# Kernel tuning notes

Measured on AMD Instinct MI355X. Metric: run time of the kernel, lower is better.

Reference implementation:

```python
import jax, jax.numpy as jnp
import numpy as np

D_MODEL = 1024
NUM_HEADS = 16
HEAD_DIM = D_MODEL // NUM_HEADS


def setup_inputs() -> dict:
    key = jax.random.key(0)
    ks = jax.random.split(key, 7)
    B, S = 4, 2048
    scale = 1.0 / np.sqrt(D_MODEL)
    x = jax.random.normal(ks[0], (B, S, D_MODEL), dtype=jnp.float32)
    Wq = jax.random.normal(ks[1], (D_MODEL, D_MODEL), dtype=jnp.float32) * scale
    Wk = jax.random.normal(ks[2], (D_MODEL, D_MODEL), dtype=jnp.float32) * scale
    Wv = jax.random.normal(ks[3], (D_MODEL, D_MODEL), dtype=jnp.float32) * scale
    bq = jax.random.normal(ks[4], (D_MODEL,), dtype=jnp.float32) * 0.02
    bk = jax.random.normal(ks[5], (D_MODEL,), dtype=jnp.float32) * 0.02
    bv = jax.random.normal(ks[6], (D_MODEL,), dtype=jnp.float32) * 0.02
    return {"x": x, "Wq": Wq, "bq": bq, "Wk": Wk, "bk": bk, "Wv": Wv, "bv": bv}


def reference(x, Wq, bq, Wk, bk, Wv, bv):
    B, S, _ = x.shape
    # QKV projections (nn.Linear: x @ W^T + b; here W stored as [in, out] already)
    q = x @ Wq + bq
    k = x @ Wk + bk
    v = x @ Wv + bv
    # [B, H, S, Dh]
    def split_heads(t):
        return t.reshape(B, S, NUM_HEADS, HEAD_DIM).transpose(0, 2, 1, 3)
    q, k, v = split_heads(q), split_heads(k), split_heads(v)
    # NOTE: module scales by sqrt(d_model), NOT sqrt(head_dim)
    scores = jnp.einsum("bhqd,bhkd->bhqk", q, k) / jnp.sqrt(jnp.float32(D_MODEL))
    attn = jax.nn.softmax(scores, axis=-1)  # dropout = identity (eval mode)
    out = jnp.einsum("bhqk,bhkd->bhqd", attn, v)
    return out.transpose(0, 2, 1, 3).reshape(B, S, D_MODEL)
```

## Files before the change

### kernel.cpp

```cpp
#include <hip/hip_runtime.h>


typedef __attribute__((ext_vector_type(8))) __bf16 bf16x8;
typedef __attribute__((ext_vector_type(8))) unsigned short ushort8;
typedef __attribute__((ext_vector_type(4))) float floatx4;

#if __has_builtin(__builtin_amdgcn_exp2f)
#define EXP2(x) __builtin_amdgcn_exp2f(x)
#else
#define EXP2(x) __expf((x) * 0.6931471805599453f)
#endif

__device__ __forceinline__ unsigned short f2bf(float f) {
    __bf16 h = (__bf16)f;
    return __builtin_bit_cast(unsigned short, h);
}
__device__ __forceinline__ bf16x8 pack8(floatx4 a, floatx4 b) {
    bf16x8 v = {(__bf16)a[0], (__bf16)a[1], (__bf16)a[2], (__bf16)a[3],
                (__bf16)b[0], (__bf16)b[1], (__bf16)b[2], (__bf16)b[3]};
    return v;
}
__device__ __forceinline__ floatx4 mfma16(bf16x8 a, bf16x8 b, floatx4 c) {
    return __builtin_amdgcn_mfma_f32_16x16x32_bf16(a, b, c, 0, 0, 0);
}
__device__ __forceinline__ int spos(int s) {
    int rk = s & 31;
    return (s & ~31) | (((rk & 15) >> 2) * 8 + ((rk >> 4) << 2) + (rk & 3));
}
__device__ __forceinline__ void glds16(const void* g, void* l) {
    __builtin_amdgcn_global_load_lds(
        (const __attribute__((address_space(1))) unsigned int*)g,
        (__attribute__((address_space(3))) unsigned int*)l, 16, 0, 0);
}

__global__ __launch_bounds__(256) void prep_x(const float* __restrict__ X,
                                              unsigned short* __restrict__ Xb) {
    int i = (blockIdx.x * 256 + threadIdx.x) * 8;
    float4 a = *(const float4*)&X[i];
    float4 b = *(const float4*)&X[i + 4];
    bf16x8 v = {(__bf16)a.x, (__bf16)a.y, (__bf16)a.z, (__bf16)a.w,
                (__bf16)b.x, (__bf16)b.y, (__bf16)b.z, (__bf16)b.w};
    *(bf16x8*)&Xb[i] = v;
}

__global__ __launch_bounds__(256) void prep_wt(
    const float* __restrict__ Wq, const float* __restrict__ Wk,
    const float* __restrict__ Wv,
    unsigned short* __restrict__ WqT, unsigned short* __restrict__ WkT,
    unsigned short* __restrict__ WvT) {
    __shared__ unsigned short Ls[64 * 72];
    const int tid = threadIdx.x, z = blockIdx.z;
    const float* W = (z == 0) ? Wq : (z == 1) ? Wk : Wv;
    unsigned short* WT = (z == 0) ? WqT : (z == 1) ? WkT : WvT;
    const int k0 = (blockIdx.x >> 4) * 64, o0 = (blockIdx.x & 15) * 64;
#pragma unroll
    for (int e = 0; e < 4; ++e) {
        int idx = e * 256 + tid;
        int r = idx >> 4, c = (idx & 15) * 4;
        float4 f = *(const float4*)&W[(size_t)(k0 + r) * 1024 + o0 + c];
        Ls[(c + 0) * 72 + r] = f2bf(f.x);
        Ls[(c + 1) * 72 + r] = f2bf(f.y);
        Ls[(c + 2) * 72 + r] = f2bf(f.z);
        Ls[(c + 3) * 72 + r] = f2bf(f.w);
    }
    __syncthreads();
#pragma unroll
    for (int e = 0; e < 2; ++e) {
        int idx = e * 256 + tid;
        int rr = idx >> 3, ch = (idx & 7) * 8;
        *(ushort8*)&WT[(size_t)(o0 + rr) * 1024 + k0 + ch] =
            *(const ushort8*)&Ls[rr * 72 + ch];
    }
}

__global__ __launch_bounds__(256, 3) void qkv_gemm(
    const unsigned short* __restrict__ Xb,
    const unsigned short* __restrict__ WqT,
    const unsigned short* __restrict__ WkT,
    const unsigned short* __restrict__ WvT,
    const float* __restrict__ bq, const float* __restrict__ bk,
    const float* __restrict__ bv,
    unsigned short* __restrict__ Kh, unsigned short* __restrict__ Vt,
    float* __restrict__ Qs_out) {

    __shared__ __align__(16) unsigned char arena[32768];

    const int tid = threadIdx.x;
    const int w = tid >> 6, lane = tid & 63;
    const int l15 = lane & 15, quad = lane >> 4;
    const int z = blockIdx.z;
    const int tok_base = blockIdx.x * 128, o_base = blockIdx.y * 128;
    const int wr = w >> 1, wc = w & 1;

    const unsigned short* Wsrc = (z == 0) ? WkT : (z == 1) ? WvT : WqT;
    const char* Asrc = (z == 1) ? (const char*)(Wsrc + (size_t)o_base * 1024)
                                : (const char*)(Xb + (size_t)tok_base * 1024);
    const char* Bsrc = (z == 1) ? (const char*)(Xb + (size_t)tok_base * 1024)
                                : (const char*)(Wsrc + (size_t)o_base * 1024);

    const int coff = (((lane & 7) ^ (lane >> 3)) << 4);
    const char* pa[4];
    const char* pb[4];
    unsigned char* la[4];
    unsigned char* lb[4];
#pragma unroll
    for (int e = 0; e < 4; ++e) {
        int r = (e * 4 + w) * 8 + (lane >> 3);
        pa[e] = Asrc + (size_t)r * 2048 + coff;
        pb[e] = Bsrc + (size_t)r * 2048 + coff;
        la[e] = arena + (e * 4 + w) * 1024;
        lb[e] = arena + 16384 + (e * 4 + w) * 1024;
    }

    const unsigned cq = (unsigned)((quad ^ (l15 & 7)) << 4);
    unsigned offA[4], offB[4];
#pragma unroll
    for (int t = 0; t < 4; ++t) {
        offA[t] = (unsigned)((wr * 64 + t * 16 + l15) * 128) + cq;
        offB[t] = 16384u + (unsigned)((wc * 64 + t * 16 + l15) * 128) + cq;
    }

    floatx4 acc[4][4];
#pragma unroll
    for (int mt = 0; mt < 4; ++mt)
#pragma unroll
        for (int nt = 0; nt < 4; ++nt) acc[mt][nt] = (floatx4){0.f, 0.f, 0.f, 0.f};

    for (int k0 = 0; k0 < 1024; k0 += 64) {
        __syncthreads();
#pragma unroll
        for (int e = 0; e < 4; ++e) {
            glds16(pa[e], la[e]);
            glds16(pb[e], lb[e]);
            pa[e] += 128;
            pb[e] += 128;
        }
        __syncthreads();

#pragma unroll
        for (int kc = 0; kc < 2; ++kc) {
            bf16x8 af[4], bfr[4];
#pragma unroll
            for (int mt = 0; mt < 4; ++mt)
                af[mt] = *(const bf16x8*)&arena[offA[mt] ^ (unsigned)(kc << 6)];
#pragma unroll
            for (int nt = 0; nt < 4; ++nt)
                bfr[nt] = *(const bf16x8*)&arena[offB[nt] ^ (unsigned)(kc << 6)];
#pragma unroll
            for (int mt = 0; mt < 4; ++mt)
#pragma unroll
                for (int nt = 0; nt < 4; ++nt)
                    acc[mt][nt] = mfma16(af[mt], bfr[nt], acc[mt][nt]);
        }
    }

    if (z == 0) {
#pragma unroll
        for (int nt = 0; nt < 4; ++nt) {
            int col = o_base + wc * 64 + nt * 16 + l15;
            float bia = bk[col];
            int h = col >> 6, dh = col & 63;
#pragma unroll
            for (int mt = 0; mt < 4; ++mt)
#pragma unroll
                for (int r = 0; r < 4; ++r) {
                    int t = tok_base + wr * 64 + mt * 16 + quad * 4 + r;
                    int bb = t >> 11, s = t & 2047;
                    Kh[(((size_t)(bb * 16 + h)) * 2048 + s) * 64 + dh] =
                        f2bf(acc[mt][nt][r] + bia);
                }
        }
    } else if (z == 1) {
#pragma unroll
        for (int mt = 0; mt < 4; ++mt)
#pragma unroll
            for (int r = 0; r < 4; ++r) {
                int o = o_base + wr * 64 + mt * 16 + quad * 4 + r;
                float bia = bv[o];
#pragma unroll
                for (int nt = 0; nt < 4; ++nt) {
                    int t = tok_base + wc * 64 + nt * 16 + l15;
                    int bb = t >> 11, s = t & 2047;
                    Vt[((size_t)(bb * 1024 + o)) * 2048 + spos(s)] =
                        f2bf(acc[mt][nt][r] + bia);
                }
            }
    } else {
        const float QS = 0.03125f * 1.44269504f;
#pragma unroll
        for (int nt = 0; nt < 4; ++nt) {
            int col = o_base + wc * 64 + nt * 16 + l15;
            float bia = bq[col];
#pragma unroll
            for (int mt = 0; mt < 4; ++mt)
#pragma unroll
                for (int r = 0; r < 4; ++r) {
                    int t = tok_base + wr * 64 + mt * 16 + quad * 4 + r;
                    Qs_out[(size_t)t * 1024 + col] = (acc[mt][nt][r] + bia) * QS;
                }
        }
    }
}

__global__ __launch_bounds__(256, 4) void attn_kernel(
    const unsigned short* __restrict__ Kh,
    const unsigned short* __restrict__ Vt,
    float* __restrict__ out) {

    __shared__ __align__(16) unsigned char arena[32768];

    const int tid = threadIdx.x;
    const int w = tid >> 6, lane = tid & 63;
    const int l15 = lane & 15, quad = lane >> 4;
    const int qb = blockIdx.x, h = blockIdx.y, b = blockIdx.z;
    const size_t head_elems = ((size_t)(b * 16 + h)) * 2048 * 64;

    bf16x8 aq[2][2];
#pragma unroll
    for (int g = 0; g < 2; ++g)
#pragma unroll
        for (int kc = 0; kc < 2; ++kc) {
            const float* qp = out +
                (size_t)(b * 2048 + qb * 128 + w * 32 + g * 16 + l15) * 1024 +
                h * 64 + kc * 32 + quad * 8;
            floatx4 x0 = *(const floatx4*)qp;
            floatx4 x1 = *(const floatx4*)(qp + 4);
            aq[g][kc] = pack8(x0, x1);
        }
    __builtin_amdgcn_sched_barrier(0);

    const int coff = (((lane & 7) ^ (lane >> 3)) << 4);
    const char* pk[2];
    const char* pv[2];
    unsigned char* lk[2];
    unsigned char* lv[2];
#pragma unroll
    for (int e = 0; e < 2; ++e) {
        int r = (e * 4 + w) * 8 + (lane >> 3);
        pk[e] = (const char*)Kh + head_elems * 2 + (size_t)r * 128 + coff;
        pv[e] = (const char*)Vt + ((size_t)(b * 1024 + h * 64 + r)) * 4096 + coff;
        lk[e] = arena + (e * 4 + w) * 1024;
        lv[e] = arena + 8192 + (e * 4 + w) * 1024;
    }
    auto stage = [&](int bufsel) {
        int bo = bufsel << 14;
#pragma unroll
        for (int e = 0; e < 2; ++e) {
            glds16(pk[e], lk[e] + bo);
            glds16(pv[e], lv[e] + bo);
            pk[e] += 8192;
            pv[e] += 128;
        }
    };

    unsigned kb[4], vb[4];
#pragma unroll
    for (int t = 0; t < 4; ++t) {
        int rk = t * 16 + l15;
        unsigned sw = (unsigned)((quad ^ (rk & 7)) << 4);
        kb[t] = (unsigned)(rk * 128) + sw;
        vb[t] = 8192u + (unsigned)(rk * 128) + sw;
    }

    float l_part[2] = {0.f, 0.f};
    floatx4 O[2][4];
#pragma unroll
    for (int g = 0; g < 2; ++g)
#pragma unroll
        for (int n4 = 0; n4 < 4; ++n4) O[g][n4] = (floatx4){0.f, 0.f, 0.f, 0.f};

    stage(0);

#pragma unroll 1
    for (int kt = 0; kt < 32; ++kt) {
        if (kt < 31) {
            stage((kt + 1) & 1);
            asm volatile("s_waitcnt vmcnt(4)" ::: "memory");
        } else {
            asm volatile("s_waitcnt vmcnt(0)" ::: "memory");
        }
        __builtin_amdgcn_s_barrier();
        const unsigned bsel = (unsigned)((kt & 1) << 14);

        bf16x8 ap[2][2];
#pragma unroll
        for (int kg = 0; kg < 2; ++kg) {
            floatx4 s0[2], s1[2];
#pragma unroll
            for (int mm = 0; mm < 2; ++mm) {
                int m16 = 2 * kg + mm;
                unsigned ka = kb[m16] ^ bsel;
                bf16x8 kf0 = *(const bf16x8*)&arena[ka];
                bf16x8 kf1 = *(const bf16x8*)&arena[ka ^ 64u];
#pragma unroll
                for (int g = 0; g < 2; ++g) {
                    floatx4 a0 = (floatx4){0.f, 0.f, 0.f, 0.f};
                    a0 = mfma16(kf0, aq[g][0], a0);
                    a0 = mfma16(kf1, aq[g][1], a0);
                    if (mm == 0) s0[g] = a0; else s1[g] = a0;
                }
            }
#pragma unroll
            for (int g = 0; g < 2; ++g) {
                floatx4 p0, p1;
#pragma unroll
                for (int r = 0; r < 4; ++r) {
                    p0[r] = EXP2(fminf(s0[g][r], 43.28f));
                    p1[r] = EXP2(fminf(s1[g][r], 43.28f));
                }
                l_part[g] += (p0[0] + p0[1]) + (p0[2] + p0[3]) +
                             (p1[0] + p1[1]) + (p1[2] + p1[3]);
                ap[g][kg] = pack8(p0, p1);
            }
        }

#pragma unroll
        for (int n4 = 0; n4 < 4; ++n4)
#pragma unroll
            for (int kg = 0; kg < 2; ++kg) {
                bf16x8 vf = *(const bf16x8*)
                    &arena[(vb[n4] ^ bsel) ^ (unsigned)(kg << 6)];
#pragma unroll
                for (int g = 0; g < 2; ++g)
                    O[g][n4] = mfma16(ap[g][kg], vf, O[g][n4]);
            }

        asm volatile("s_waitcnt lgkmcnt(0)" ::: "memory");
        __builtin_amdgcn_s_barrier();
    }

#pragma unroll
    for (int g = 0; g < 2; ++g) {
        float l = l_part[g];
        l += __shfl_xor(l, 16);
        l += __shfl_xor(l, 32);
#pragma unroll
        for (int r = 0; r < 4; ++r) {
            float lr = __shfl(l, (lane & 48) | (quad * 4 + r));
            float inv = 1.f / lr;
            int srow = qb * 128 + w * 32 + g * 16 + quad * 4 + r;
#pragma unroll
            for (int n4 = 0; n4 < 4; ++n4)
                out[((size_t)(b * 2048 + srow)) * 1024 + h * 64 + n4 * 16 + l15] =
                    O[g][n4][r] * inv;
        }
    }
}

extern "C" void kernel_launch(void* const* d_in, const int* in_sizes, int n_in,
                              void* d_out, int out_size, void* d_ws, size_t ws_size,
                              hipStream_t stream) {
    const float *x, *Wq, *bq, *Wk, *bk, *Wv, *bv;
    x = (const float*)d_in[0];
    if (in_sizes[2] == 1024) {
        Wq = (const float*)d_in[1];  bq = (const float*)d_in[2];
        Wk = (const float*)d_in[3];  bk = (const float*)d_in[4];
        Wv = (const float*)d_in[5];  bv = (const float*)d_in[6];
    } else {
        Wq = (const float*)d_in[1];  Wk = (const float*)d_in[2];
        Wv = (const float*)d_in[3];
        bq = (const float*)d_in[4];  bk = (const float*)d_in[5];
        bv = (const float*)d_in[6];
    }
    float* out = (float*)d_out;

    char* ws = (char*)d_ws;
    unsigned short* Xb  = (unsigned short*)(ws);
    unsigned short* Kh  = (unsigned short*)(ws + (16u << 20));
    unsigned short* Vt  = (unsigned short*)(ws + (32u << 20));
    unsigned short* WqT = (unsigned short*)(ws + (48u << 20));
    unsigned short* WkT = (unsigned short*)(ws + (50u << 20));
    unsigned short* WvT = (unsigned short*)(ws + (52u << 20));

    prep_x<<<4096, 256, 0, stream>>>(x, Xb);
    prep_wt<<<dim3(256, 1, 3), 256, 0, stream>>>(Wq, Wk, Wv, WqT, WkT, WvT);
    qkv_gemm<<<dim3(64, 8, 3), 256, 0, stream>>>(Xb, WqT, WkT, WvT, bq, bk, bv,
                                                 Kh, Vt, out);
    attn_kernel<<<dim3(16, 16, 4), 256, 0, stream>>>(Kh, Vt, out);
}
```

Measured before the change: 232.0 us.

## Merge prep kernels, compute softmax row sums via MFMA, add wave priorities

Folds the x conversion and weight transpose kernels into one launch split by block index, removing a kernel boundary. In attention, the per-row sum of exponentials now comes from an MFMA against a ones vector on the bf16-packed probabilities instead of scalar adds plus cross-lane shuffles. It also wraps the MFMA sections in s_setprio and drops the fminf clamp before exp2. Removing the clamp risks overflow if scores get large, and summing bf16-rounded probabilities slightly changes the normalisation.

```diff
diff --git a/kernel.cpp b/kernel.cpp
--- a/kernel.cpp
+++ b/kernel.cpp
@@ -33,26 +33,28 @@
         (__attribute__((address_space(3))) unsigned int*)l, 16, 0, 0);
 }
 
-__global__ __launch_bounds__(256) void prep_x(const float* __restrict__ X,
-                                              unsigned short* __restrict__ Xb) {
-    int i = (blockIdx.x * 256 + threadIdx.x) * 8;
-    float4 a = *(const float4*)&X[i];
-    float4 b = *(const float4*)&X[i + 4];
-    bf16x8 v = {(__bf16)a.x, (__bf16)a.y, (__bf16)a.z, (__bf16)a.w,
-                (__bf16)b.x, (__bf16)b.y, (__bf16)b.z, (__bf16)b.w};
-    *(bf16x8*)&Xb[i] = v;
-}
-
-__global__ __launch_bounds__(256) void prep_wt(
+__global__ __launch_bounds__(256) void prep_all(
+    const float* __restrict__ X, unsigned short* __restrict__ Xb,
     const float* __restrict__ Wq, const float* __restrict__ Wk,
     const float* __restrict__ Wv,
     unsigned short* __restrict__ WqT, unsigned short* __restrict__ WkT,
     unsigned short* __restrict__ WvT) {
     __shared__ unsigned short Ls[64 * 72];
-    const int tid = threadIdx.x, z = blockIdx.z;
+    const int tid = threadIdx.x, bx = blockIdx.x;
+    if (bx < 4096) {
+        int i = (bx * 256 + tid) * 8;
+        float4 a = *(const float4*)&X[i];
+        float4 b = *(const float4*)&X[i + 4];
+        bf16x8 v = {(__bf16)a.x, (__bf16)a.y, (__bf16)a.z, (__bf16)a.w,
+                    (__bf16)b.x, (__bf16)b.y, (__bf16)b.z, (__bf16)b.w};
+        *(bf16x8*)&Xb[i] = v;
+        return;
+    }
+    const int idx4 = bx - 4096;
+    const int z = idx4 >> 8, xx = idx4 & 255;
     const float* W = (z == 0) ? Wq : (z == 1) ? Wk : Wv;
     unsigned short* WT = (z == 0) ? WqT : (z == 1) ? WkT : WvT;
-    const int k0 = (blockIdx.x >> 4) * 64, o0 = (blockIdx.x & 15) * 64;
+    const int k0 = (xx >> 4) * 64, o0 = (xx & 15) * 64;
 #pragma unroll
     for (int e = 0; e < 4; ++e) {
         int idx = e * 256 + tid;
@@ -262,12 +264,16 @@
         vb[t] = 8192u + (unsigned)(rk * 128) + sw;
     }
 
-    float l_part[2] = {0.f, 0.f};
+    const bf16x8 ONES = {(__bf16)1.f, (__bf16)1.f, (__bf16)1.f, (__bf16)1.f,
+                         (__bf16)1.f, (__bf16)1.f, (__bf16)1.f, (__bf16)1.f};
+    floatx4 lacc[2];
     floatx4 O[2][4];
 #pragma unroll
-    for (int g = 0; g < 2; ++g)
+    for (int g = 0; g < 2; ++g) {
+        lacc[g] = (floatx4){0.f, 0.f, 0.f, 0.f};
 #pragma unroll
         for (int n4 = 0; n4 < 4; ++n4) O[g][n4] = (floatx4){0.f, 0.f, 0.f, 0.f};
+    }
 
     stage(0);
 
@@ -286,6 +292,7 @@
 #pragma unroll
         for (int kg = 0; kg < 2; ++kg) {
             floatx4 s0[2], s1[2];
+            __builtin_amdgcn_s_setprio(1);
 #pragma unroll
             for (int mm = 0; mm < 2; ++mm) {
                 int m16 = 2 * kg + mm;
@@ -300,20 +307,21 @@
                     if (mm == 0) s0[g] = a0; else s1[g] = a0;
                 }
             }
+            __builtin_amdgcn_s_setprio(0);
 #pragma unroll
             for (int g = 0; g < 2; ++g) {
                 floatx4 p0, p1;
 #pragma unroll
                 for (int r = 0; r < 4; ++r) {
-                    p0[r] = EXP2(fminf(s0[g][r], 43.28f));
-                    p1[r] = EXP2(fminf(s1[g][r], 43.28f));
-                }
-                l_part[g] += (p0[0] + p0[1]) + (p0[2] + p0[3]) +
-                             (p1[0] + p1[1]) + (p1[2] + p1[3]);
+                    p0[r] = EXP2(s0[g][r]);
+                    p1[r] = EXP2(s1[g][r]);
+                }
                 ap[g][kg] = pack8(p0, p1);
+                lacc[g] = mfma16(ap[g][kg], ONES, lacc[g]);
             }
         }
 
+        __builtin_amdgcn_s_setprio(1);
 #pragma unroll
         for (int n4 = 0; n4 < 4; ++n4)
 #pragma unroll
@@ -324,27 +332,23 @@
                 for (int g = 0; g < 2; ++g)
                     O[g][n4] = mfma16(ap[g][kg], vf, O[g][n4]);
             }
+        __builtin_amdgcn_s_setprio(0);
 
         asm volatile("s_waitcnt lgkmcnt(0)" ::: "memory");
         __builtin_amdgcn_s_barrier();
     }
 
 #pragma unroll
-    for (int g = 0; g < 2; ++g) {
-        float l = l_part[g];
-        l += __shfl_xor(l, 16);
-        l += __shfl_xor(l, 32);
+    for (int g = 0; g < 2; ++g)
 #pragma unroll
         for (int r = 0; r < 4; ++r) {
-            float lr = __shfl(l, (lane & 48) | (quad * 4 + r));
-            float inv = 1.f / lr;
+            float inv = 1.f / lacc[g][r];
             int srow = qb * 128 + w * 32 + g * 16 + quad * 4 + r;
 #pragma unroll
             for (int n4 = 0; n4 < 4; ++n4)
                 out[((size_t)(b * 2048 + srow)) * 1024 + h * 64 + n4 * 16 + l15] =
                     O[g][n4][r] * inv;
         }
-    }
 }
 
 extern "C" void kernel_launch(void* const* d_in, const int* in_sizes, int n_in,
@@ -372,8 +376,7 @@
     unsigned short* WkT = (unsigned short*)(ws + (50u << 20));
     unsigned short* WvT = (unsigned short*)(ws + (52u << 20));
 
-    prep_x<<<4096, 256, 0, stream>>>(x, Xb);
-    prep_wt<<<dim3(256, 1, 3), 256, 0, stream>>>(Wq, Wk, Wv, WqT, WkT, WvT);
+    prep_all<<<4864, 256, 0, stream>>>(x, Xb, Wq, Wk, Wv, WqT, WkT, WvT);
     qkv_gemm<<<dim3(64, 8, 3), 256, 0, stream>>>(Xb, WqT, WkT, WvT, bq, bk, bv,
                                                  Kh, Vt, out);
     attn_kernel<<<dim3(16, 16, 4), 256, 0, stream>>>(Kh, Vt, out);
```

Measured after the change: 221.4 us. 4.6% less time.
